# Optimization experiments

Measured on AMD Instinct MI355X. Metric: run time of the kernel, lower is better.

Reference implementation:

```python
import jax, jax.numpy as jnp
import numpy as np

NUM_HEADS = 16
HEAD_DIM = 64
QUERY_DIM = 1024
CONTEXT_DIM = 1024
PROJ_DIM = NUM_HEADS * HEAD_DIM
SCALE = HEAD_DIM ** -0.5


def setup_inputs() -> dict:
    key = jax.random.key(0)
    ks = jax.random.split(key, 6)
    B, Lq, Lkv = 4, 1024, 2048
    query = jax.random.normal(ks[0], (B, Lq, QUERY_DIM), dtype=jnp.float32)
    context = jax.random.normal(ks[1], (B, Lkv, CONTEXT_DIM), dtype=jnp.float32)
    # Learned params (Linear weights stored as [in, out] for x @ W)
    Wq = jax.random.normal(ks[2], (QUERY_DIM, PROJ_DIM), dtype=jnp.float32) * 0.02
    Wkv = jax.random.normal(ks[3], (CONTEXT_DIM, 2 * PROJ_DIM), dtype=jnp.float32) * 0.02
    Wo = jax.random.normal(ks[4], (PROJ_DIM, QUERY_DIM), dtype=jnp.float32) * 0.02
    bo = jax.random.normal(ks[5], (QUERY_DIM,), dtype=jnp.float32) * 0.02
    return {"query": query, "context": context, "Wq": Wq, "Wkv": Wkv, "Wo": Wo, "bo": bo}


def reference(query, context, Wq, Wkv, Wo, bo):
    B, Lq, _ = query.shape
    q = query @ Wq                      # [B, Lq, n*d]
    kv = context @ Wkv                  # [B, Lkv, 2*n*d]
    k, v = jnp.split(kv, 2, axis=-1)

    def split_heads(t):
        b, l, _ = t.shape
        return t.reshape(b, l, NUM_HEADS, HEAD_DIM).transpose(0, 2, 1, 3)  # [B, n, L, d]

    q, k, v = map(split_heads, (q, k, v))
    # dot-product attention scores
    attn = jnp.einsum('bnid,bnjd->bnij', q, k) * SCALE
    attn = jax.nn.softmax(attn, axis=-1)            # [B, n, Lq, Lkv]
    out = jnp.einsum('bnij,bnjd->bnid', attn, v)    # [B, n, Lq, d]
    out = out.transpose(0, 2, 1, 3).reshape(B, Lq, PROJ_DIM)
    out = out @ Wo + bo                              # [B, Lq, query_dim]
    # original returns attn as [(B*n), Lq, Lkv]
    attn_flat = attn.reshape(B * NUM_HEADS, Lq, attn.shape[-1])
    return out, attn_flat
```

## Files before the change

kernel.cpp:

```cpp
#include <hip/hip_runtime.h>
#include <stdint.h>


typedef unsigned short ushort_t;
typedef __bf16 bf16x8 __attribute__((ext_vector_type(8)));
typedef float  f32x4  __attribute__((ext_vector_type(4)));
typedef ushort_t u16x8 __attribute__((ext_vector_type(8)));

__device__ __forceinline__ float bf2f(ushort_t h) {
  union { unsigned int u; float f; } c; c.u = ((unsigned int)h) << 16; return c.f;
}
__device__ __forceinline__ ushort_t f2bf(float f) {
  union { float f; unsigned int u; } c; c.f = f;
  unsigned int u = c.u;
  return (ushort_t)((u + 0x7FFFu + ((u >> 16) & 1u)) >> 16);
}

__global__ void wconv_t(const float* __restrict__ in, ushort_t* __restrict__ out,
                        int ldi, int ldo) {
  __shared__ ushort_t t[32][33];
  const int r0 = blockIdx.y * 32, c0 = blockIdx.x * 32;
  const int tx = threadIdx.x & 31, ty = threadIdx.x >> 5;
#pragma unroll
  for (int i = 0; i < 4; i++) {
    int r = ty + i * 8;
    t[r][tx] = f2bf(in[(long)(r0 + r) * ldi + c0 + tx]);
  }
  __syncthreads();
#pragma unroll
  for (int i = 0; i < 4; i++) {
    int c = ty + i * 8;
    out[(long)(c0 + c) * ldo + r0 + tx] = t[tx][c];
  }
}

__global__ void transpose_bf16(const ushort_t* __restrict__ in,
                               ushort_t* __restrict__ out, int ldi, int ldo) {
  __shared__ ushort_t t[32][33];
  const int r0 = blockIdx.y * 32, c0 = blockIdx.x * 32;
  const int tx = threadIdx.x & 31, ty = threadIdx.x >> 5;
#pragma unroll
  for (int i = 0; i < 4; i++) {
    int r = ty + i * 8;
    t[r][tx] = in[(long)(r0 + r) * ldi + c0 + tx];
  }
  __syncthreads();
#pragma unroll
  for (int i = 0; i < 4; i++) {
    int c = ty + i * 8;
    out[(long)(c0 + c) * ldo + r0 + tx] = t[tx][c];
  }
}

#define GLDT 72

template <bool AF32, bool CF32>
__global__ __launch_bounds__(256, 2) void gemm_bt(
    const void* __restrict__ Ap, const ushort_t* __restrict__ Bt,
    void* __restrict__ Cp, const float* __restrict__ bias,
    int K, int lda, int ldb, int ldc) {
  __shared__ ushort_t As[128 * GLDT];
  __shared__ ushort_t Bs[128 * GLDT];
  const int tid  = threadIdx.x;
  const int wave = tid >> 6, lane = tid & 63;
  const int quad = lane >> 4, l15 = lane & 15;
  const int wr = wave >> 1, wc = wave & 1;
  const long m0 = (long)blockIdx.x * 128;
  const long n0 = (long)blockIdx.y * 128;
  const int ar = tid >> 3;
  const int ac = (tid & 7) * 8;

  f32x4 acc[4][4];
#pragma unroll
  for (int i = 0; i < 4; i++)
#pragma unroll
    for (int j = 0; j < 4; j++) acc[i][j] = (f32x4)0.0f;

  for (int k0 = 0; k0 < K; k0 += 64) {
    __syncthreads();
#pragma unroll
    for (int p = 0; p < 4; p++) {
      int row = p * 32 + ar;
      if (AF32) {
        const float* A = (const float*)Ap;
        f32x4 x0 = *(const f32x4*)(&A[(m0 + row) * lda + k0 + ac]);
        f32x4 x1 = *(const f32x4*)(&A[(m0 + row) * lda + k0 + ac + 4]);
        u16x8 v;
#pragma unroll
        for (int e = 0; e < 4; e++) { v[e] = f2bf(x0[e]); v[4 + e] = f2bf(x1[e]); }
        *(u16x8*)(&As[row * GLDT + ac]) = v;
      } else {
        const ushort_t* A = (const ushort_t*)Ap;
        *(u16x8*)(&As[row * GLDT + ac]) =
            *(const u16x8*)(&A[(m0 + row) * lda + k0 + ac]);
      }
      *(u16x8*)(&Bs[row * GLDT + ac]) =
          *(const u16x8*)(&Bt[(n0 + row) * ldb + k0 + ac]);
    }
    __syncthreads();
#pragma unroll
    for (int ks = 0; ks < 64; ks += 32) {
      bf16x8 af[4], bfr[4];
#pragma unroll
      for (int i = 0; i < 4; i++)
        af[i] = *(const bf16x8*)(&As[(wr * 64 + i * 16 + l15) * GLDT + ks + quad * 8]);
#pragma unroll
      for (int j = 0; j < 4; j++)
        bfr[j] = *(const bf16x8*)(&Bs[(wc * 64 + j * 16 + l15) * GLDT + ks + quad * 8]);
#pragma unroll
      for (int i = 0; i < 4; i++)
#pragma unroll
        for (int j = 0; j < 4; j++)
          acc[i][j] = __builtin_amdgcn_mfma_f32_16x16x32_bf16(af[i], bfr[j], acc[i][j], 0, 0, 0);
    }
  }
#pragma unroll
  for (int i = 0; i < 4; i++) {
    long row = m0 + wr * 64 + i * 16 + quad * 4;
#pragma unroll
    for (int j = 0; j < 4; j++) {
      long col = n0 + wc * 64 + j * 16 + l15;
      float bv = bias ? bias[col] : 0.0f;
#pragma unroll
      for (int r = 0; r < 4; r++) {
        float v = acc[i][j][r] + bv;
        if (CF32) ((float*)Cp)[(row + r) * ldc + col] = v;
        else      ((ushort_t*)Cp)[(row + r) * ldc + col] = f2bf(v);
      }
    }
  }
}

#define LQK 72
#define LPJ 136

__global__ __launch_bounds__(256, 2) void attn_kernel(
    const ushort_t* __restrict__ qb,
    const ushort_t* __restrict__ kb,
    const ushort_t* __restrict__ vt,
    float* __restrict__ pout,
    ushort_t* __restrict__ ao) {
  __shared__ ushort_t Qs[64 * LQK];
  __shared__ ushort_t Ks[128 * LQK];
  __shared__ ushort_t Vs[64 * LPJ];
  __shared__ ushort_t Ps[64 * LPJ];

  const int tid  = threadIdx.x;
  const int wave = tid >> 6, lane = tid & 63;
  const int quad = lane >> 4, l15 = lane & 15;
  const int bn = blockIdx.x;
  const int b = bn >> 4, h = bn & 15;
  const int q0 = blockIdx.y * 64;
  const float SL2E = 0.125f * 1.44269504088896340736f;

  {
    int r = tid >> 3, c = (tid & 7) * 8;
#pragma unroll
    for (int p = 0; p < 2; p++) {
      int row = p * 32 + r;
      *(u16x8*)(&Qs[row * LQK + c]) =
          *(const u16x8*)(&qb[((long)(b * 1024 + q0 + row)) * 1024 + h * 64 + c]);
    }
  }
  __syncthreads();
  bf16x8 aq0 = *(const bf16x8*)(&Qs[(wave * 16 + l15) * LQK + quad * 8]);
  bf16x8 aq1 = *(const bf16x8*)(&Qs[(wave * 16 + l15) * LQK + 32 + quad * 8]);

  float m[4], l[4];
#pragma unroll
  for (int r = 0; r < 4; r++) { m[r] = -1e30f; l[r] = 0.0f; }

  for (int t0 = 0; t0 < 2048; t0 += 128) {
    __syncthreads();
    {
      int r = tid >> 3, c = (tid & 7) * 8;
#pragma unroll
      for (int p = 0; p < 4; p++) {
        int row = p * 32 + r;
        *(u16x8*)(&Ks[row * LQK + c]) =
            *(const u16x8*)(&kb[((long)(b * 2048 + t0 + row)) * 1024 + h * 64 + c]);
      }
    }
    __syncthreads();
    float u[8][4];
#pragma unroll
    for (int ni = 0; ni < 8; ni++) {
      bf16x8 b0 = *(const bf16x8*)(&Ks[(ni * 16 + l15) * LQK + quad * 8]);
      bf16x8 b1 = *(const bf16x8*)(&Ks[(ni * 16 + l15) * LQK + 32 + quad * 8]);
      f32x4 s = (f32x4)0.0f;
      s = __builtin_amdgcn_mfma_f32_16x16x32_bf16(aq0, b0, s, 0, 0, 0);
      s = __builtin_amdgcn_mfma_f32_16x16x32_bf16(aq1, b1, s, 0, 0, 0);
#pragma unroll
      for (int r = 0; r < 4; r++) u[ni][r] = s[r] * SL2E;
    }
#pragma unroll
    for (int r = 0; r < 4; r++) {
      float tm = u[0][r];
#pragma unroll
      for (int ni = 1; ni < 8; ni++) tm = fmaxf(tm, u[ni][r]);
      tm = fmaxf(tm, __shfl_xor(tm, 1));
      tm = fmaxf(tm, __shfl_xor(tm, 2));
      tm = fmaxf(tm, __shfl_xor(tm, 4));
      tm = fmaxf(tm, __shfl_xor(tm, 8));
      float mn = fmaxf(m[r], tm);
      float ts = 0.0f;
#pragma unroll
      for (int ni = 0; ni < 8; ni++) ts += __builtin_amdgcn_exp2f(u[ni][r] - mn);
      ts += __shfl_xor(ts, 1);
      ts += __shfl_xor(ts, 2);
      ts += __shfl_xor(ts, 4);
      ts += __shfl_xor(ts, 8);
      l[r] = l[r] * __builtin_amdgcn_exp2f(m[r] - mn) + ts;
      m[r] = mn;
    }
  }

  float rl[4];
#pragma unroll
  for (int r = 0; r < 4; r++) rl[r] = 1.0f / l[r];

  f32x4 o[4];
#pragma unroll
  for (int d = 0; d < 4; d++) o[d] = (f32x4)0.0f;

  for (int t0 = 0; t0 < 2048; t0 += 128) {
    __syncthreads();
    {
      int r = tid >> 3, c = (tid & 7) * 8;
#pragma unroll
      for (int p = 0; p < 4; p++) {
        int row = p * 32 + r;
        *(u16x8*)(&Ks[row * LQK + c]) =
            *(const u16x8*)(&kb[((long)(b * 2048 + t0 + row)) * 1024 + h * 64 + c]);
      }
      int r2 = tid >> 4, c2 = (tid & 15) * 8;
#pragma unroll
      for (int p = 0; p < 4; p++) {
        int row = p * 16 + r2;
        *(u16x8*)(&Vs[row * LPJ + c2]) =
            *(const u16x8*)(&vt[((long)(bn * 64 + row)) * 2048 + t0 + c2]);
      }
    }
    __syncthreads();
#pragma unroll
    for (int ni = 0; ni < 8; ni++) {
      bf16x8 b0 = *(const bf16x8*)(&Ks[(ni * 16 + l15) * LQK + quad * 8]);
      bf16x8 b1 = *(const bf16x8*)(&Ks[(ni * 16 + l15) * LQK + 32 + quad * 8]);
      f32x4 s = (f32x4)0.0f;
      s = __builtin_amdgcn_mfma_f32_16x16x32_bf16(aq0, b0, s, 0, 0, 0);
      s = __builtin_amdgcn_mfma_f32_16x16x32_bf16(aq1, b1, s, 0, 0, 0);
#pragma unroll
      for (int r = 0; r < 4; r++) {
        float pv = __builtin_amdgcn_exp2f(s[r] * SL2E - m[r]) * rl[r];
        Ps[(wave * 16 + quad * 4 + r) * LPJ + ni * 16 + l15] = f2bf(pv);
      }
    }
    __syncthreads();
    {
      int r = tid >> 4, c = (tid & 15) * 8;
#pragma unroll
      for (int p = 0; p < 4; p++) {
        int row = p * 16 + r;
        const ushort_t* src = &Ps[row * LPJ + c];
        float* dst = &pout[((long)bn * 1024 + q0 + row) * 2048 + t0 + c];
        f32x4 lo, hi;
#pragma unroll
        for (int e = 0; e < 4; e++) { lo[e] = bf2f(src[e]); hi[e] = bf2f(src[4 + e]); }
        *(f32x4*)dst = lo;
        *(f32x4*)(dst + 4) = hi;
      }
    }
#pragma unroll
    for (int js = 0; js < 128; js += 32) {
      bf16x8 ap = *(const bf16x8*)(&Ps[(wave * 16 + l15) * LPJ + js + quad * 8]);
#pragma unroll
      for (int d = 0; d < 4; d++) {
        bf16x8 bv = *(const bf16x8*)(&Vs[(d * 16 + l15) * LPJ + js + quad * 8]);
        o[d] = __builtin_amdgcn_mfma_f32_16x16x32_bf16(ap, bv, o[d], 0, 0, 0);
      }
    }
  }
#pragma unroll
  for (int d = 0; d < 4; d++) {
#pragma unroll
    for (int r = 0; r < 4; r++) {
      int row = q0 + wave * 16 + quad * 4 + r;
      int col = h * 64 + d * 16 + l15;
      ao[((long)(b * 1024 + row)) * 1024 + col] = f2bf(o[d][r]);
    }
  }
}

extern "C" void kernel_launch(void* const* d_in, const int* in_sizes, int n_in,
                              void* d_out, int out_size, void* d_ws, size_t ws_size,
                              hipStream_t stream) {
  (void)in_sizes; (void)n_in; (void)out_size; (void)ws_size;
  const float* query   = (const float*)d_in[0];
  const float* context = (const float*)d_in[1];
  const float* Wq      = (const float*)d_in[2];
  const float* Wkv     = (const float*)d_in[3];
  const float* Wo      = (const float*)d_in[4];
  const float* bo      = (const float*)d_in[5];
  float* out = (float*)d_out;

  char* ws = (char*)d_ws;
  ushort_t* WoT  = (ushort_t*)(ws);
  ushort_t* WqT  = (ushort_t*)(ws + (2ll  << 20));
  ushort_t* WkvT = (ushort_t*)(ws + (4ll  << 20));
  ushort_t* qbuf = (ushort_t*)(ws + (8ll  << 20));
  ushort_t* kbuf = (ushort_t*)(ws + (16ll << 20));
  ushort_t* vbuf = (ushort_t*)(ws + (32ll << 20));
  ushort_t* vt   = (ushort_t*)(ws + (48ll << 20));
  ushort_t* ao   = vbuf;

  wconv_t<<<dim3(32, 32), 256, 0, stream>>>(Wq, WqT, 1024, 1024);
  wconv_t<<<dim3(64, 32), 256, 0, stream>>>(Wkv, WkvT, 2048, 1024);
  wconv_t<<<dim3(32, 32), 256, 0, stream>>>(Wo, WoT, 1024, 1024);

  gemm_bt<true, false><<<dim3(32, 8), 256, 0, stream>>>(
      query, WqT, qbuf, nullptr, 1024, 1024, 1024, 1024);
  gemm_bt<true, false><<<dim3(64, 8), 256, 0, stream>>>(
      context, WkvT, kbuf, nullptr, 1024, 1024, 1024, 1024);
  gemm_bt<true, false><<<dim3(64, 8), 256, 0, stream>>>(
      context, WkvT + 1024ll * 1024, vbuf, nullptr, 1024, 1024, 1024, 1024);

  for (int b = 0; b < 4; b++)
    transpose_bf16<<<dim3(32, 64), 256, 0, stream>>>(
        vbuf + (long)b * 2048 * 1024, vt + (long)b * 1024 * 2048, 1024, 2048);

  attn_kernel<<<dim3(64, 16), 256, 0, stream>>>(qbuf, kbuf, vt, out + 4194304, ao);

  gemm_bt<false, true><<<dim3(32, 8), 256, 0, stream>>>(
      ao, WoT, out, bo, 1024, 1024, 1024, 1024);
}
```

Before: 946.7 us.

## Use direct global-to-LDS loads with XOR swizzle and pre-convert activations to bf16

```diff
diff --git a/kernel.cpp b/kernel.cpp
--- a/kernel.cpp
+++ b/kernel.cpp
@@ -5,7 +5,7 @@
 typedef unsigned short ushort_t;
 typedef __bf16 bf16x8 __attribute__((ext_vector_type(8)));
 typedef float  f32x4  __attribute__((ext_vector_type(4)));
-typedef ushort_t u16x8 __attribute__((ext_vector_type(8)));
+typedef unsigned short u16x8 __attribute__((ext_vector_type(8)));
 
 __device__ __forceinline__ float bf2f(ushort_t h) {
   union { unsigned int u; float f; } c; c.u = ((unsigned int)h) << 16; return c.f;
@@ -14,6 +14,22 @@
   union { float f; unsigned int u; } c; c.f = f;
   unsigned int u = c.u;
   return (ushort_t)((u + 0x7FFFu + ((u >> 16) & 1u)) >> 16);
+}
+
+__device__ __forceinline__ void gl16(const void* gp, void* lp) {
+  __builtin_amdgcn_global_load_lds(
+      (__attribute__((address_space(1))) void*)(void*)gp,
+      (__attribute__((address_space(3))) void*)lp, 16, 0, 0);
+}
+
+__global__ void cvt_bf16(const float* __restrict__ in, ushort_t* __restrict__ out) {
+  long i = ((long)blockIdx.x * 256 + threadIdx.x) * 8;
+  f32x4 a = *(const f32x4*)(&in[i]);
+  f32x4 b = *(const f32x4*)(&in[i + 4]);
+  u16x8 v;
+#pragma unroll
+  for (int e = 0; e < 4; e++) { v[e] = f2bf(a[e]); v[4 + e] = f2bf(b[e]); }
+  *(u16x8*)(&out[i]) = v;
 }
 
 __global__ void wconv_t(const float* __restrict__ in, ushort_t* __restrict__ out,
@@ -35,8 +51,11 @@
 }
 
 __global__ void transpose_bf16(const ushort_t* __restrict__ in,
-                               ushort_t* __restrict__ out, int ldi, int ldo) {
+                               ushort_t* __restrict__ out, int ldi, int ldo,
+                               long sbi, long sbo) {
   __shared__ ushort_t t[32][33];
+  in += (long)blockIdx.z * sbi;
+  out += (long)blockIdx.z * sbo;
   const int r0 = blockIdx.y * 32, c0 = blockIdx.x * 32;
   const int tx = threadIdx.x & 31, ty = threadIdx.x >> 5;
 #pragma unroll
@@ -52,23 +71,21 @@
   }
 }
 
-#define GLDT 72
-
-template <bool AF32, bool CF32>
+template <bool CF32>
 __global__ __launch_bounds__(256, 2) void gemm_bt(
-    const void* __restrict__ Ap, const ushort_t* __restrict__ Bt,
+    const ushort_t* __restrict__ A, const ushort_t* __restrict__ Bt,
     void* __restrict__ Cp, const float* __restrict__ bias,
     int K, int lda, int ldb, int ldc) {
-  __shared__ ushort_t As[128 * GLDT];
-  __shared__ ushort_t Bs[128 * GLDT];
+  __shared__ ushort_t As[128 * 64];
+  __shared__ ushort_t Bs[128 * 64];
   const int tid  = threadIdx.x;
   const int wave = tid >> 6, lane = tid & 63;
   const int quad = lane >> 4, l15 = lane & 15;
   const int wr = wave >> 1, wc = wave & 1;
   const long m0 = (long)blockIdx.x * 128;
   const long n0 = (long)blockIdx.y * 128;
-  const int ar = tid >> 3;
-  const int ac = (tid & 7) * 8;
+  const int srow = tid >> 3;
+  const int scol = (((tid & 7) ^ (srow & 7)) & 7) << 3;
 
   f32x4 acc[4][4];
 #pragma unroll
@@ -79,34 +96,28 @@
   for (int k0 = 0; k0 < K; k0 += 64) {
     __syncthreads();
 #pragma unroll
-    for (int p = 0; p < 4; p++) {
-      int row = p * 32 + ar;
-      if (AF32) {
-        const float* A = (const float*)Ap;
-        f32x4 x0 = *(const f32x4*)(&A[(m0 + row) * lda + k0 + ac]);
-        f32x4 x1 = *(const f32x4*)(&A[(m0 + row) * lda + k0 + ac + 4]);
-        u16x8 v;
-#pragma unroll
-        for (int e = 0; e < 4; e++) { v[e] = f2bf(x0[e]); v[4 + e] = f2bf(x1[e]); }
-        *(u16x8*)(&As[row * GLDT + ac]) = v;
-      } else {
-        const ushort_t* A = (const ushort_t*)Ap;
-        *(u16x8*)(&As[row * GLDT + ac]) =
-            *(const u16x8*)(&A[(m0 + row) * lda + k0 + ac]);
-      }
-      *(u16x8*)(&Bs[row * GLDT + ac]) =
-          *(const u16x8*)(&Bt[(n0 + row) * ldb + k0 + ac]);
+    for (int i = 0; i < 4; i++) {
+      int row = i * 32 + srow;
+      gl16(&A [(m0 + row) * lda + k0 + scol], (char*)As + i * 4096 + tid * 16);
+      gl16(&Bt[(n0 + row) * ldb + k0 + scol], (char*)Bs + i * 4096 + tid * 16);
     }
     __syncthreads();
 #pragma unroll
     for (int ks = 0; ks < 64; ks += 32) {
+      const int gb = ks >> 3;
       bf16x8 af[4], bfr[4];
 #pragma unroll
-      for (int i = 0; i < 4; i++)
-        af[i] = *(const bf16x8*)(&As[(wr * 64 + i * 16 + l15) * GLDT + ks + quad * 8]);
-#pragma unroll
-      for (int j = 0; j < 4; j++)
-        bfr[j] = *(const bf16x8*)(&Bs[(wc * 64 + j * 16 + l15) * GLDT + ks + quad * 8]);
+      for (int i = 0; i < 4; i++) {
+        int row = wr * 64 + i * 16 + l15;
+        af[i] = *(const bf16x8*)((const char*)As + (row << 7) +
+                                 ((((gb + quad) ^ (row & 7)) & 7) << 4));
+      }
+#pragma unroll
+      for (int j = 0; j < 4; j++) {
+        int row = wc * 64 + j * 16 + l15;
+        bfr[j] = *(const bf16x8*)((const char*)Bs + (row << 7) +
+                                  ((((gb + quad) ^ (row & 7)) & 7) << 4));
+      }
 #pragma unroll
       for (int i = 0; i < 4; i++)
 #pragma unroll
@@ -141,8 +152,8 @@
     float* __restrict__ pout,
     ushort_t* __restrict__ ao) {
   __shared__ ushort_t Qs[64 * LQK];
-  __shared__ ushort_t Ks[128 * LQK];
-  __shared__ ushort_t Vs[64 * LPJ];
+  __shared__ ushort_t Ks[128 * 64];
+  __shared__ ushort_t Vs[64 * 128];
   __shared__ ushort_t Ps[64 * LPJ];
 
   const int tid  = threadIdx.x;
@@ -153,6 +164,11 @@
   const int q0 = blockIdx.y * 64;
   const float SL2E = 0.125f * 1.44269504088896340736f;
 
+  const int srow = tid >> 3;
+  const int scol = (((tid & 7) ^ (srow & 7)) & 7) << 3;
+  const int vrs  = tid >> 4;
+  const int vcs  = (((tid & 15) ^ vrs) & 15) << 3;
+
   {
     int r = tid >> 3, c = (tid & 7) * 8;
 #pragma unroll
@@ -172,21 +188,21 @@
 
   for (int t0 = 0; t0 < 2048; t0 += 128) {
     __syncthreads();
-    {
-      int r = tid >> 3, c = (tid & 7) * 8;
-#pragma unroll
-      for (int p = 0; p < 4; p++) {
-        int row = p * 32 + r;
-        *(u16x8*)(&Ks[row * LQK + c]) =
-            *(const u16x8*)(&kb[((long)(b * 2048 + t0 + row)) * 1024 + h * 64 + c]);
-      }
+#pragma unroll
+    for (int i = 0; i < 4; i++) {
+      int row = i * 32 + srow;
+      gl16(&kb[((long)(b * 2048 + t0 + row)) * 1024 + h * 64 + scol],
+           (char*)Ks + i * 4096 + tid * 16);
     }
     __syncthreads();
     float u[8][4];
 #pragma unroll
     for (int ni = 0; ni < 8; ni++) {
-      bf16x8 b0 = *(const bf16x8*)(&Ks[(ni * 16 + l15) * LQK + quad * 8]);
-      bf16x8 b1 = *(const bf16x8*)(&Ks[(ni * 16 + l15) * LQK + 32 + quad * 8]);
+      int krow = ni * 16 + l15;
+      bf16x8 b0 = *(const bf16x8*)((const char*)Ks + (krow << 7) +
+                                   (((quad ^ (krow & 7)) & 7) << 4));
+      bf16x8 b1 = *(const bf16x8*)((const char*)Ks + (krow << 7) +
+                                   ((((4 + quad) ^ (krow & 7)) & 7) << 4));
       f32x4 s = (f32x4)0.0f;
       s = __builtin_amdgcn_mfma_f32_16x16x32_bf16(aq0, b0, s, 0, 0, 0);
       s = __builtin_amdgcn_mfma_f32_16x16x32_bf16(aq1, b1, s, 0, 0, 0);
@@ -223,59 +239,45 @@
 #pragma unroll
   for (int d = 0; d < 4; d++) o[d] = (f32x4)0.0f;
 
+  const long pbase = ((long)bn * 1024 + q0 + wave * 16 + quad * 4) * 2048 + l15;
   for (int t0 = 0; t0 < 2048; t0 += 128) {
     __syncthreads();
-    {
-      int r = tid >> 3, c = (tid & 7) * 8;
-#pragma unroll
-      for (int p = 0; p < 4; p++) {
-        int row = p * 32 + r;
-        *(u16x8*)(&Ks[row * LQK + c]) =
-            *(const u16x8*)(&kb[((long)(b * 2048 + t0 + row)) * 1024 + h * 64 + c]);
-      }
-      int r2 = tid >> 4, c2 = (tid & 15) * 8;
-#pragma unroll
-      for (int p = 0; p < 4; p++) {
-        int row = p * 16 + r2;
-        *(u16x8*)(&Vs[row * LPJ + c2]) =
-            *(const u16x8*)(&vt[((long)(bn * 64 + row)) * 2048 + t0 + c2]);
-      }
+#pragma unroll
+    for (int i = 0; i < 4; i++) {
+      int row = i * 32 + srow;
+      gl16(&kb[((long)(b * 2048 + t0 + row)) * 1024 + h * 64 + scol],
+           (char*)Ks + i * 4096 + tid * 16);
+      int vr = i * 16 + vrs;
+      gl16(&vt[((long)(bn * 64 + vr)) * 2048 + t0 + vcs],
+           (char*)Vs + i * 4096 + tid * 16);
     }
     __syncthreads();
 #pragma unroll
     for (int ni = 0; ni < 8; ni++) {
-      bf16x8 b0 = *(const bf16x8*)(&Ks[(ni * 16 + l15) * LQK + quad * 8]);
-      bf16x8 b1 = *(const bf16x8*)(&Ks[(ni * 16 + l15) * LQK + 32 + quad * 8]);
+      int krow = ni * 16 + l15;
+      bf16x8 b0 = *(const bf16x8*)((const char*)Ks + (krow << 7) +
+                                   (((quad ^ (krow & 7)) & 7) << 4));
+      bf16x8 b1 = *(const bf16x8*)((const char*)Ks + (krow << 7) +
+                                   ((((4 + quad) ^ (krow & 7)) & 7) << 4));
       f32x4 s = (f32x4)0.0f;
       s = __builtin_amdgcn_mfma_f32_16x16x32_bf16(aq0, b0, s, 0, 0, 0);
       s = __builtin_amdgcn_mfma_f32_16x16x32_bf16(aq1, b1, s, 0, 0, 0);
 #pragma unroll
       for (int r = 0; r < 4; r++) {
         float pv = __builtin_amdgcn_exp2f(s[r] * SL2E - m[r]) * rl[r];
+        pout[pbase + (long)r * 2048 + t0 + ni * 16] = pv;
         Ps[(wave * 16 + quad * 4 + r) * LPJ + ni * 16 + l15] = f2bf(pv);
       }
     }
-    __syncthreads();
-    {
-      int r = tid >> 4, c = (tid & 15) * 8;
-#pragma unroll
-      for (int p = 0; p < 4; p++) {
-        int row = p * 16 + r;
-        const ushort_t* src = &Ps[row * LPJ + c];
-        float* dst = &pout[((long)bn * 1024 + q0 + row) * 2048 + t0 + c];
-        f32x4 lo, hi;
-#pragma unroll
-        for (int e = 0; e < 4; e++) { lo[e] = bf2f(src[e]); hi[e] = bf2f(src[4 + e]); }
-        *(f32x4*)dst = lo;
-        *(f32x4*)(dst + 4) = hi;
-      }
-    }
 #pragma unroll
     for (int js = 0; js < 128; js += 32) {
+      const int gb = js >> 3;
       bf16x8 ap = *(const bf16x8*)(&Ps[(wave * 16 + l15) * LPJ + js + quad * 8]);
 #pragma unroll
       for (int d = 0; d < 4; d++) {
-        bf16x8 bv = *(const bf16x8*)(&Vs[(d * 16 + l15) * LPJ + js + quad * 8]);
+        int vrow = d * 16 + l15;
+        bf16x8 bv = *(const bf16x8*)((const char*)Vs + (vrow << 8) +
+                                     ((((gb + quad) ^ l15) & 15) << 4));
         o[d] = __builtin_amdgcn_mfma_f32_16x16x32_bf16(ap, bv, o[d], 0, 0, 0);
       }
     }
@@ -309,27 +311,31 @@
   ushort_t* WkvT = (ushort_t*)(ws + (4ll  << 20));
   ushort_t* qbuf = (ushort_t*)(ws + (8ll  << 20));
   ushort_t* kbuf = (ushort_t*)(ws + (16ll << 20));
-  ushort_t* vbuf = (ushort_t*)(ws + (32ll << 20));
-  ushort_t* vt   = (ushort_t*)(ws + (48ll << 20));
-  ushort_t* ao   = vbuf;
+  ushort_t* cbf  = (ushort_t*)(ws + (32ll << 20));
+  ushort_t* vt   = (ushort_t*)(ws + (32ll << 20));
+  ushort_t* qbf  = (ushort_t*)(ws + (48ll << 20));
+  ushort_t* vbuf = (ushort_t*)(ws + (48ll << 20));
+  ushort_t* ao   = (ushort_t*)(ws + (48ll << 20));
 
   wconv_t<<<dim3(32, 32), 256, 0, stream>>>(Wq, WqT, 1024, 1024);
   wconv_t<<<dim3(64, 32), 256, 0, stream>>>(Wkv, WkvT, 2048, 1024);
   wconv_t<<<dim3(32, 32), 256, 0, stream>>>(Wo, WoT, 1024, 1024);
 
-  gemm_bt<true, false><<<dim3(32, 8), 256, 0, stream>>>(
-      query, WqT, qbuf, nullptr, 1024, 1024, 1024, 1024);
-  gemm_bt<true, false><<<dim3(64, 8), 256, 0, stream>>>(
-      context, WkvT, kbuf, nullptr, 1024, 1024, 1024, 1024);
-  gemm_bt<true, false><<<dim3(64, 8), 256, 0, stream>>>(
-      context, WkvT + 1024ll * 1024, vbuf, nullptr, 1024, 1024, 1024, 1024);
-
-  for (int b = 0; b < 4; b++)
-    transpose_bf16<<<dim3(32, 64), 256, 0, stream>>>(
-        vbuf + (long)b * 2048 * 1024, vt + (long)b * 1024 * 2048, 1024, 2048);
+  cvt_bf16<<<2048, 256, 0, stream>>>(query, qbf);
+  cvt_bf16<<<4096, 256, 0, stream>>>(context, cbf);
+
+  gemm_bt<false><<<dim3(32, 8), 256, 0, stream>>>(
+      qbf, WqT, qbuf, nullptr, 1024, 1024, 1024, 1024);
+  gemm_bt<false><<<dim3(64, 8), 256, 0, stream>>>(
+      cbf, WkvT, kbuf, nullptr, 1024, 1024, 1024, 1024);
+  gemm_bt<false><<<dim3(64, 8), 256, 0, stream>>>(
+      cbf, WkvT + 1024ll * 1024, vbuf, nullptr, 1024, 1024, 1024, 1024);
+
+  transpose_bf16<<<dim3(32, 64, 4), 256, 0, stream>>>(
+      vbuf, vt, 1024, 2048, 2048ll * 1024, 1024ll * 2048);
 
   attn_kernel<<<dim3(64, 16), 256, 0, stream>>>(qbuf, kbuf, vt, out + 4194304, ao);
 
-  gemm_bt<false, true><<<dim3(32, 8), 256, 0, stream>>>(
+  gemm_bt<true><<<dim3(32, 8), 256, 0, stream>>>(
       ao, WoT, out, bo, 1024, 1024, 1024, 1024);
 }
```

After: 788.2 us. -16.7%, faster.
